# Performance work log

Measured on AMD Instinct MI355X. Metric: run time of the kernel, lower is better.

The kernel has to match this reference:

```python
import jax, jax.numpy as jnp
import numpy as np


def setup_inputs() -> dict:
    key = jax.random.key(0)
    k1, k2 = jax.random.split(key)
    x = jax.random.normal(k1, (8, 512, 32, 14, 14), dtype=jnp.float32)
    # Conv1d(in=1, out=1, kernel=5, bias=False) weight, torch layout (O, I, K)
    conv_w = jax.random.normal(k2, (1, 1, 5), dtype=jnp.float32) * 0.2
    return {"x": x, "conv_w": conv_w}


def reference(x, conv_w):
    # x: (N, C, T, H, W)
    N, C, T = x.shape[:3]
    PAD = 2  # k=5, padding=k//2
    # Global average pool over H, W -> (N, C, T)
    gap = x.mean(axis=(3, 4))
    # Original loops over T applying Conv1d over the channel axis per timestep.
    # Batched equivalent: fold T into the batch dim -> (N*T, 1, C)
    seq = gap.transpose(0, 2, 1).reshape(N * T, 1, C)
    y = jax.lax.conv_general_dilated(
        seq, conv_w, window_strides=(1,), padding=[(PAD, PAD)],
        dimension_numbers=("NCH", "OIH", "NCH"))  # (N*T, 1, C)
    att = jax.nn.sigmoid(y.reshape(N, T, C).transpose(0, 2, 1))  # (N, C, T)
    return att[..., None, None]  # (N, C, T, 1, 1)
```

## Files before the change

kernel.cpp:

```cpp
#include <hip/hip_runtime.h>
#include <hip/hip_bf16.h>


#define ROWS_PER_BLOCK 64
#define F4_PER_ROW 49
#define F4_PER_BLOCK (ROWS_PER_BLOCK * F4_PER_ROW)
#define THREADS_A 256

__global__ __launch_bounds__(THREADS_A) void gap_kernel(
        const float* __restrict__ x,
        float* __restrict__ gap) {
    __shared__ float part[F4_PER_BLOCK];

    const int tid = threadIdx.x;
    const float4* p = reinterpret_cast<const float4*>(x) +
                      (size_t)blockIdx.x * F4_PER_BLOCK;

    #pragma unroll
    for (int j = tid; j < F4_PER_BLOCK; j += THREADS_A) {
        float4 v = p[j];
        part[j] = (v.x + v.y) + (v.z + v.w);
    }
    __syncthreads();

    if (tid < ROWS_PER_BLOCK) {
        const float* q = &part[tid * F4_PER_ROW];
        float s = 0.0f;
        #pragma unroll
        for (int k = 0; k < F4_PER_ROW; ++k) s += q[k];
        gap[(size_t)blockIdx.x * ROWS_PER_BLOCK + tid] = s * (1.0f / 196.0f);
    }
}

__global__ void conv_sig_kernel(const float* __restrict__ gap,
                                const float* __restrict__ w,
                                float* __restrict__ out,
                                int N, int C, int T) {
    const int idx = blockIdx.x * blockDim.x + threadIdx.x;
    const int total = N * C * T;
    if (idx >= total) return;

    const int t = idx % T;
    const int c = (idx / T) % C;
    const int n = idx / (T * C);

    const float w0 = w[0], w1 = w[1], w2 = w[2], w3 = w[3], w4 = w[4];

    const float* g = gap + ((size_t)n * C) * T + t;
    float acc = w2 * g[c * T];
    if (c >= 2)      acc += w0 * g[(c - 2) * T];
    if (c >= 1)      acc += w1 * g[(c - 1) * T];
    if (c + 1 < C)   acc += w3 * g[(c + 1) * T];
    if (c + 2 < C)   acc += w4 * g[(c + 2) * T];

    out[idx] = 1.0f / (1.0f + __expf(-acc));
}

extern "C" void kernel_launch(void* const* d_in, const int* in_sizes, int n_in,
                              void* d_out, int out_size, void* d_ws, size_t ws_size,
                              hipStream_t stream) {
    const float* x = (const float*)d_in[0];
    const float* w = (const float*)d_in[1];
    float* out = (float*)d_out;
    float* gap = (float*)d_ws;

    const int N = 8, C = 512, T = 32;
    const int total_rows = N * C * T;
    const int blocksA = total_rows / ROWS_PER_BLOCK;

    gap_kernel<<<blocksA, THREADS_A, 0, stream>>>(x, gap);

    const int threadsB = 256;
    const int blocksB = (total_rows + threadsB - 1) / threadsB;
    conv_sig_kernel<<<blocksB, threadsB, 0, stream>>>(gap, w, out, N, C, T);
}
```

Measured before the change: 24.25 us.

## Reduce GAP rows with 4 threads per row and warp shuffles instead of LDS

Each block still covers 64 rows, but now four lanes share each row. Every lane strides through that row's float4s and accumulates in registers, and the four partial sums are combined with xor shuffles. This removes the shared-memory staging buffer, the barrier, and the serial 49-element summation done by 64 threads. In exchange, each lane's loads are strided by 4 float4s, so a wavefront's accesses span 16 rows, which can lower coalescing efficiency, and the leftover 49th float4 of each row is read by only one lane.

```diff
diff --git a/kernel.cpp b/kernel.cpp
--- a/kernel.cpp
+++ b/kernel.cpp
@@ -10,26 +10,33 @@
 __global__ __launch_bounds__(THREADS_A) void gap_kernel(
         const float* __restrict__ x,
         float* __restrict__ gap) {
-    __shared__ float part[F4_PER_BLOCK];
+    const int tid = threadIdx.x;
+    const int s = tid >> 2;
+    const int q = tid & 3;
 
-    const int tid = threadIdx.x;
     const float4* p = reinterpret_cast<const float4*>(x) +
-                      (size_t)blockIdx.x * F4_PER_BLOCK;
+                      (size_t)blockIdx.x * F4_PER_BLOCK + s * F4_PER_ROW + q;
 
+    float4 a0 = p[0];
+    float4 a1 = p[4];
     #pragma unroll
-    for (int j = tid; j < F4_PER_BLOCK; j += THREADS_A) {
-        float4 v = p[j];
-        part[j] = (v.x + v.y) + (v.z + v.w);
+    for (int i = 2; i < 12; i += 2) {
+        float4 u = p[4 * i];
+        float4 w = p[4 * (i + 1)];
+        a0.x += u.x; a0.y += u.y; a0.z += u.z; a0.w += u.w;
+        a1.x += w.x; a1.y += w.y; a1.z += w.z; a1.w += w.w;
     }
-    __syncthreads();
+    float sum = ((a0.x + a1.x) + (a0.y + a1.y)) + ((a0.z + a1.z) + (a0.w + a1.w));
+    if (q == 0) {
+        float4 u = p[48];
+        sum += (u.x + u.y) + (u.z + u.w);
+    }
 
-    if (tid < ROWS_PER_BLOCK) {
-        const float* q = &part[tid * F4_PER_ROW];
-        float s = 0.0f;
-        #pragma unroll
-        for (int k = 0; k < F4_PER_ROW; ++k) s += q[k];
-        gap[(size_t)blockIdx.x * ROWS_PER_BLOCK + tid] = s * (1.0f / 196.0f);
-    }
+    sum += __shfl_xor(sum, 1, 64);
+    sum += __shfl_xor(sum, 2, 64);
+
+    if (q == 0)
+        gap[(size_t)blockIdx.x * ROWS_PER_BLOCK + s] = sum * (1.0f / 196.0f);
 }
 
 __global__ void conv_sig_kernel(const float* __restrict__ gap,
```

Result: faster. 23.31 us (-3.9%).
